# Kernel tuning notes

Measured on AMD Instinct MI355X. Metric: run time of the kernel, lower is better.

The kernel has to match this reference:

```python
import jax, jax.numpy as jnp
import numpy as np


def _lstm(x_seq, Wih, Whh, bih, bhh, hidden):
    """Single-layer batch_first LSTM, PyTorch gate order (i,f,g,o).
    x_seq: [B, T, D_in]. Returns (outputs [B, T, H], h_T [B, H])."""
    B = x_seq.shape[0]
    h0 = jnp.zeros((B, hidden), x_seq.dtype)
    c0 = jnp.zeros((B, hidden), x_seq.dtype)

    def step(carry, x_t):
        h, c = carry
        gates = x_t @ Wih.T + bih + h @ Whh.T + bhh  # [B, 4H]
        i, f, g, o = jnp.split(gates, 4, axis=-1)
        i = jax.nn.sigmoid(i)
        f = jax.nn.sigmoid(f)
        g = jnp.tanh(g)
        o = jax.nn.sigmoid(o)
        c = f * c + i * g
        h = o * jnp.tanh(c)
        return (h, c), h

    (hT, _), hs = jax.lax.scan(step, (h0, c0), jnp.swapaxes(x_seq, 0, 1))
    return jnp.swapaxes(hs, 0, 1), hT


def setup_inputs() -> dict:
    key = jax.random.key(0)
    ks = jax.random.split(key, 20)
    B, T = 4096, 140
    W = 0.1  # weight scale to keep gates out of saturation
    inp = {"x": jax.random.normal(ks[0], (B, 1, T), jnp.float32)}
    shapes = {
        "Wih_e1": (512, 1), "Whh_e1": (512, 128), "bih_e1": (512,), "bhh_e1": (512,),
        "Wih_e2": (256, 128), "Whh_e2": (256, 64), "bih_e2": (256,), "bhh_e2": (256,),
        "Wih_d1": (512, 64), "Whh_d1": (512, 128), "bih_d1": (512,), "bhh_d1": (512,),
        "Wih_d2": (4, 128), "Whh_d2": (4, 1), "bih_d2": (4,), "bhh_d2": (4,),
    }
    for i, (name, shp) in enumerate(shapes.items()):
        inp[name] = jax.random.normal(ks[i + 1], shp, jnp.float32) * W
    return inp


def reference(x, Wih_e1, Whh_e1, bih_e1, bhh_e1,
              Wih_e2, Whh_e2, bih_e2, bhh_e2,
              Wih_d1, Whh_d1, bih_d1, bhh_d1,
              Wih_d2, Whh_d2, bih_d2, bhh_d2):
    T = 140
    # x: [B,1,140] -> [B,140,1]
    x_enc = x[:, 0, :, None]
    _, h1 = _lstm(x_enc, Wih_e1, Whh_e1, bih_e1, bhh_e1, 128)  # h1: [B,128]
    # faithful to original bug: hn1 [1,B,128] fed as batch_first input (batch=1, seq=B)
    hn1_seq = h1[None, :, :]
    _, z = _lstm(hn1_seq, Wih_e2, Whh_e2, bih_e2, bhh_e2, 64)  # z: [1,64]
    dec_in = jnp.broadcast_to(z[:, None, :], (1, T, 64))
    out1, _ = _lstm(dec_in, Wih_d1, Whh_d1, bih_d1, bhh_d1, 128)  # [1,140,128]
    out2, _ = _lstm(out1, Wih_d2, Whh_d2, bih_d2, bhh_d2, 1)      # [1,140,1]
    recon = out2[..., 0][:, None, :]  # [1,1,140]
    return recon
```

## Files before the change

kernel.cpp:

```cpp
#include <hip/hip_runtime.h>
#include <hip/hip_bf16.h>


__device__ __forceinline__ float sigm(float x) {
  return 1.0f / (1.0f + __expf(-x));
}
__device__ __forceinline__ float tanh_fast(float x) {
  return 1.0f - 2.0f / (__expf(2.0f * x) + 1.0f);
}

template <int IMM>
__device__ __forceinline__ float qp(float v) {
  return __int_as_float(__builtin_amdgcn_ds_swizzle(__float_as_int(v), IMM));
}
#define QP_XOR1 0x80B1
#define QP_XOR2 0x804E
#define QP_ROT1 0x8093

__device__ __forceinline__ int swzc(int k) { return k + ((k >> 5) << 2); }

#define A_BB 16

__global__ __launch_bounds__(512, 2) void lstm_e1_kernel(
    const float* __restrict__ x,
    const float* __restrict__ Wih,
    const float* __restrict__ Whh,
    const float* __restrict__ bih,
    const float* __restrict__ bhh,
    float* __restrict__ h1_out)
{
  const int j    = threadIdx.x;
  const int lane = j & 63;
  const int w    = j >> 6;
  const int u    = w * 16 + (lane >> 2);
  const int q    = lane & 3;
  const int b0   = blockIdx.x * A_BB;

  __shared__ float Hs[2][A_BB][144];
  __shared__ float xs[2][A_BB];

  for (int i = j; i < A_BB * 144; i += 512) ((float*)Hs[0])[i] = 0.0f;
  if (j < A_BB) xs[0][j] = x[(b0 + j) * 140];

  float wr[4][32];
#pragma unroll
  for (int g = 0; g < 4; ++g)
#pragma unroll
    for (int k = 0; k < 32; k += 4)
      *(float4*)&wr[g][k] = *(const float4*)&Whh[(g * 128 + u) * 128 + q * 32 + k];

  float wih[4], bs[4];
#pragma unroll
  for (int g = 0; g < 4; ++g) {
    wih[g] = Wih[g * 128 + u];
    bs[g]  = bih[g * 128 + u] + bhh[g * 128 + u];
  }

  float c[4]  = {0.f, 0.f, 0.f, 0.f};
  float hr[4] = {0.f, 0.f, 0.f, 0.f};
  __syncthreads();

  int cur = 0;
  for (int t = 0; t < 140; ++t) {
    const int nxt = cur ^ 1;

    float R[4][4];
#pragma unroll
    for (int g = 0; g < 4; ++g)
#pragma unroll
      for (int i = 0; i < 4; ++i) R[g][i] = 0.0f;

#pragma unroll
    for (int s = 0; s < 4; ++s) {
      if (s) {
#pragma unroll
        for (int g = 0; g < 4; ++g)
#pragma unroll
          for (int i = 0; i < 4; ++i) R[g][i] = qp<QP_ROT1>(R[g][i]);
      }
      const int cch = (q - 1 - s) & 3;
      const float* hbase = &Hs[cur][cch * 4][q * 36];
#pragma unroll
      for (int i = 0; i < 4; ++i) {
        const float* hrow = hbase + i * 144;
#pragma unroll
        for (int kk = 0; kk < 8; ++kk) {
          const float4 hv = *(const float4*)&hrow[kk * 4];
#pragma unroll
          for (int g = 0; g < 4; ++g) {
            R[g][i] = __builtin_fmaf(wr[g][kk * 4 + 0], hv.x, R[g][i]);
            R[g][i] = __builtin_fmaf(wr[g][kk * 4 + 1], hv.y, R[g][i]);
            R[g][i] = __builtin_fmaf(wr[g][kk * 4 + 2], hv.z, R[g][i]);
            R[g][i] = __builtin_fmaf(wr[g][kk * 4 + 3], hv.w, R[g][i]);
          }
        }
      }
    }

    if (j < A_BB && (t + 1) < 140) xs[nxt][j] = x[(b0 + j) * 140 + t + 1];

    const float4 xv = *(const float4*)&xs[cur][q * 4];
    const float xa[4] = {xv.x, xv.y, xv.z, xv.w};
#pragma unroll
    for (int i = 0; i < 4; ++i) {
      const float gi = sigm(R[0][i] + __builtin_fmaf(wih[0], xa[i], bs[0]));
      const float gf = sigm(R[1][i] + __builtin_fmaf(wih[1], xa[i], bs[1]));
      const float gg = tanh_fast(R[2][i] + __builtin_fmaf(wih[2], xa[i], bs[2]));
      const float go = sigm(R[3][i] + __builtin_fmaf(wih[3], xa[i], bs[3]));
      c[i]  = gf * c[i] + gi * gg;
      hr[i] = go * tanh_fast(c[i]);
      Hs[nxt][q * 4 + i][swzc(u)] = hr[i];
    }
    __syncthreads();
    cur = nxt;
  }

#pragma unroll
  for (int i = 0; i < 4; ++i)
    h1_out[(b0 + q * 4 + i) * 128 + u] = hr[i];
}

__global__ __launch_bounds__(256, 1) void u_pre_kernel(
    const float* __restrict__ h1,
    const float* __restrict__ Wih,
    const float* __restrict__ bih,
    const float* __restrict__ bhh,
    float* __restrict__ Up)
{
  const int t = blockIdx.x;
  const int j = threadIdx.x;
  __shared__ float hs[128];
  if (j < 128) hs[j] = h1[t * 128 + j];
  __syncthreads();
  float acc = bih[j] + bhh[j];
#pragma unroll
  for (int k = 0; k < 128; k += 4) {
    const float4 hv = *(const float4*)&hs[k];
    const float4 wv = *(const float4*)&Wih[j * 128 + k];
    acc += wv.x * hv.x + wv.y * hv.y + wv.z * hv.z + wv.w * hv.w;
  }
  Up[t * 256 + (j & 63) * 4 + (j >> 6)] = acc;
}

__global__ __launch_bounds__(256, 1) void lstm_e2_scan_kernel(
    const float4* __restrict__ Up,
    const float* __restrict__ Whh,
    float* __restrict__ z_out)
{
  const int j = threadIdx.x;
  const int u = j >> 2;
  const int q = j & 3;

  __shared__ float hb[2][64];

  float wr[4][16];
#pragma unroll
  for (int g = 0; g < 4; ++g)
#pragma unroll
    for (int k = 0; k < 16; k += 4)
      *(float4*)&wr[g][k] = *(const float4*)&Whh[(g * 64 + u) * 64 + q * 16 + k];

  if (j < 64) hb[0][j] = 0.0f;
  float c = 0.0f, h = 0.0f;

  float4 U0 = Up[u];
  float4 U1 = Up[64 + u];
  __syncthreads();

  int cur = 0;
#pragma unroll 1
  for (int t = 0; t < 4096; t += 2) {
    {
      const int tp = (t + 2 < 4096) ? (t + 2) : 4095;
      const float4 Unew = Up[tp * 64 + u];
      float a0 = 0.f, a1 = 0.f, a2 = 0.f, a3 = 0.f;
#pragma unroll
      for (int kk = 0; kk < 4; ++kk) {
        const float4 hv = *(const float4*)&hb[cur][q * 16 + kk * 4];
        a0 = __builtin_fmaf(wr[0][kk*4+0], hv.x, a0); a0 = __builtin_fmaf(wr[0][kk*4+1], hv.y, a0);
        a0 = __builtin_fmaf(wr[0][kk*4+2], hv.z, a0); a0 = __builtin_fmaf(wr[0][kk*4+3], hv.w, a0);
        a1 = __builtin_fmaf(wr[1][kk*4+0], hv.x, a1); a1 = __builtin_fmaf(wr[1][kk*4+1], hv.y, a1);
        a1 = __builtin_fmaf(wr[1][kk*4+2], hv.z, a1); a1 = __builtin_fmaf(wr[1][kk*4+3], hv.w, a1);
        a2 = __builtin_fmaf(wr[2][kk*4+0], hv.x, a2); a2 = __builtin_fmaf(wr[2][kk*4+1], hv.y, a2);
        a2 = __builtin_fmaf(wr[2][kk*4+2], hv.z, a2); a2 = __builtin_fmaf(wr[2][kk*4+3], hv.w, a2);
        a3 = __builtin_fmaf(wr[3][kk*4+0], hv.x, a3); a3 = __builtin_fmaf(wr[3][kk*4+1], hv.y, a3);
        a3 = __builtin_fmaf(wr[3][kk*4+2], hv.z, a3); a3 = __builtin_fmaf(wr[3][kk*4+3], hv.w, a3);
      }
      a0 += qp<QP_XOR1>(a0); a0 += qp<QP_XOR2>(a0);
      a1 += qp<QP_XOR1>(a1); a1 += qp<QP_XOR2>(a1);
      a2 += qp<QP_XOR1>(a2); a2 += qp<QP_XOR2>(a2);
      a3 += qp<QP_XOR1>(a3); a3 += qp<QP_XOR2>(a3);
      const float gi = sigm(a0 + U0.x);
      const float gf = sigm(a1 + U0.y);
      const float gg = tanh_fast(a2 + U0.z);
      const float go = sigm(a3 + U0.w);
      c = gf * c + gi * gg;
      h = go * tanh_fast(c);
      if (q == 0) hb[cur ^ 1][u] = h;
      U0 = Unew;
      __syncthreads();
      cur ^= 1;
    }
    {
      const int tp = (t + 3 < 4096) ? (t + 3) : 4095;
      const float4 Unew = Up[tp * 64 + u];
      float a0 = 0.f, a1 = 0.f, a2 = 0.f, a3 = 0.f;
#pragma unroll
      for (int kk = 0; kk < 4; ++kk) {
        const float4 hv = *(const float4*)&hb[cur][q * 16 + kk * 4];
        a0 = __builtin_fmaf(wr[0][kk*4+0], hv.x, a0); a0 = __builtin_fmaf(wr[0][kk*4+1], hv.y, a0);
        a0 = __builtin_fmaf(wr[0][kk*4+2], hv.z, a0); a0 = __builtin_fmaf(wr[0][kk*4+3], hv.w, a0);
        a1 = __builtin_fmaf(wr[1][kk*4+0], hv.x, a1); a1 = __builtin_fmaf(wr[1][kk*4+1], hv.y, a1);
        a1 = __builtin_fmaf(wr[1][kk*4+2], hv.z, a1); a1 = __builtin_fmaf(wr[1][kk*4+3], hv.w, a1);
        a2 = __builtin_fmaf(wr[2][kk*4+0], hv.x, a2); a2 = __builtin_fmaf(wr[2][kk*4+1], hv.y, a2);
        a2 = __builtin_fmaf(wr[2][kk*4+2], hv.z, a2); a2 = __builtin_fmaf(wr[2][kk*4+3], hv.w, a2);
        a3 = __builtin_fmaf(wr[3][kk*4+0], hv.x, a3); a3 = __builtin_fmaf(wr[3][kk*4+1], hv.y, a3);
        a3 = __builtin_fmaf(wr[3][kk*4+2], hv.z, a3); a3 = __builtin_fmaf(wr[3][kk*4+3], hv.w, a3);
      }
      a0 += qp<QP_XOR1>(a0); a0 += qp<QP_XOR2>(a0);
      a1 += qp<QP_XOR1>(a1); a1 += qp<QP_XOR2>(a1);
      a2 += qp<QP_XOR1>(a2); a2 += qp<QP_XOR2>(a2);
      a3 += qp<QP_XOR1>(a3); a3 += qp<QP_XOR2>(a3);
      const float gi = sigm(a0 + U1.x);
      const float gf = sigm(a1 + U1.y);
      const float gg = tanh_fast(a2 + U1.z);
      const float go = sigm(a3 + U1.w);
      c = gf * c + gi * gg;
      h = go * tanh_fast(c);
      if (q == 0) hb[cur ^ 1][u] = h;
      U1 = Unew;
      __syncthreads();
      cur ^= 1;
    }
  }
  if (q == 0) z_out[u] = h;
}

__global__ __launch_bounds__(512, 1) void lstm_dec_kernel(
    const float* __restrict__ z,
    const float* __restrict__ Wih1,
    const float* __restrict__ Whh1,
    const float* __restrict__ bih1,
    const float* __restrict__ bhh1,
    const float* __restrict__ Wih2,
    const float* __restrict__ Whh2,
    const float* __restrict__ bih2,
    const float* __restrict__ bhh2,
    float* __restrict__ out)
{
  const int j = threadIdx.x;
  const int u = j >> 2;
  const int q = j & 3;

  __shared__ float hb[2][144];
  __shared__ float zs[64];

  if (j < 64) zs[j] = z[j];
  if (j < 144) hb[0][j] = 0.0f;
  __syncthreads();

  float wr[4][32];
#pragma unroll
  for (int g = 0; g < 4; ++g)
#pragma unroll
    for (int k = 0; k < 32; k += 4)
      *(float4*)&wr[g][k] = *(const float4*)&Whh1[(g * 128 + u) * 128 + q * 32 + k];

  float pre0[4];
#pragma unroll
  for (int g = 0; g < 4; ++g) {
    float acc = bih1[g * 128 + u] + bhh1[g * 128 + u];
#pragma unroll
    for (int k = 0; k < 64; k += 4) {
      const float4 zv = *(const float4*)&zs[k];
      const float4 wv = *(const float4*)&Wih1[(g * 128 + u) * 64 + k];
      acc += wv.x * zv.x + wv.y * zv.y + wv.z * zv.z + wv.w * zv.w;
    }
    pre0[g] = acc;
  }

  float w2[8] = {0,0,0,0,0,0,0,0}, b2[4] = {0,0,0,0}, wh2[4] = {0,0,0,0};
  if (j < 64) {
#pragma unroll
    for (int g = 0; g < 4; ++g) {
      w2[g * 2 + 0] = Wih2[g * 128 + 2 * j + 0];
      w2[g * 2 + 1] = Wih2[g * 128 + 2 * j + 1];
      b2[g]  = bih2[g] + bhh2[g];
      wh2[g] = Whh2[g];
    }
  }

  float c1 = 0.0f;
  float c2 = 0.0f, h2 = 0.0f;

  int cur = 0;
  for (int t = 0; t < 140; ++t) {
    float a0 = 0.f, a1 = 0.f, a2 = 0.f, a3 = 0.f;
#pragma unroll
    for (int kk = 0; kk < 8; ++kk) {
      const float4 hv = *(const float4*)&hb[cur][q * 36 + kk * 4];
      a0 = __builtin_fmaf(wr[0][kk*4+0], hv.x, a0); a0 = __builtin_fmaf(wr[0][kk*4+1], hv.y, a0);
      a0 = __builtin_fmaf(wr[0][kk*4+2], hv.z, a0); a0 = __builtin_fmaf(wr[0][kk*4+3], hv.w, a0);
      a1 = __builtin_fmaf(wr[1][kk*4+0], hv.x, a1); a1 = __builtin_fmaf(wr[1][kk*4+1], hv.y, a1);
      a1 = __builtin_fmaf(wr[1][kk*4+2], hv.z, a1); a1 = __builtin_fmaf(wr[1][kk*4+3], hv.w, a1);
      a2 = __builtin_fmaf(wr[2][kk*4+0], hv.x, a2); a2 = __builtin_fmaf(wr[2][kk*4+1], hv.y, a2);
      a2 = __builtin_fmaf(wr[2][kk*4+2], hv.z, a2); a2 = __builtin_fmaf(wr[2][kk*4+3], hv.w, a2);
      a3 = __builtin_fmaf(wr[3][kk*4+0], hv.x, a3); a3 = __builtin_fmaf(wr[3][kk*4+1], hv.y, a3);
      a3 = __builtin_fmaf(wr[3][kk*4+2], hv.z, a3); a3 = __builtin_fmaf(wr[3][kk*4+3], hv.w, a3);
    }
    a0 += qp<QP_XOR1>(a0); a0 += qp<QP_XOR2>(a0);
    a1 += qp<QP_XOR1>(a1); a1 += qp<QP_XOR2>(a1);
    a2 += qp<QP_XOR1>(a2); a2 += qp<QP_XOR2>(a2);
    a3 += qp<QP_XOR1>(a3); a3 += qp<QP_XOR2>(a3);

    const float gi = sigm(a0 + pre0[0]);
    const float gf = sigm(a1 + pre0[1]);
    const float gg = tanh_fast(a2 + pre0[2]);
    const float go = sigm(a3 + pre0[3]);
    c1 = gf * c1 + gi * gg;
    const float h1v = go * tanh_fast(c1);
    if (q == 0) hb[cur ^ 1][swzc(u)] = h1v;
    __syncthreads();
    cur ^= 1;

    if (j < 64) {
      const float hA = hb[cur][swzc(2 * j)];
      const float hB = hb[cur][swzc(2 * j + 1)];
      float p0 = hA * w2[0] + hB * w2[1];
      float p1 = hA * w2[2] + hB * w2[3];
      float p2 = hA * w2[4] + hB * w2[5];
      float p3 = hA * w2[6] + hB * w2[7];
#pragma unroll
      for (int s = 1; s < 64; s <<= 1) {
        p0 += __shfl_xor(p0, s);
        p1 += __shfl_xor(p1, s);
        p2 += __shfl_xor(p2, s);
        p3 += __shfl_xor(p3, s);
      }
      const float g2i = sigm(p0 + b2[0] + wh2[0] * h2);
      const float g2f = sigm(p1 + b2[1] + wh2[1] * h2);
      const float g2g = tanh_fast(p2 + b2[2] + wh2[2] * h2);
      const float g2o = sigm(p3 + b2[3] + wh2[3] * h2);
      c2 = g2f * c2 + g2i * g2g;
      h2 = g2o * tanh_fast(c2);
      if (j == 0) out[t] = h2;
    }
  }
}

extern "C" void kernel_launch(void* const* d_in, const int* in_sizes, int n_in,
                              void* d_out, int out_size, void* d_ws, size_t ws_size,
                              hipStream_t stream) {
  const float* x      = (const float*)d_in[0];
  const float* Wih_e1 = (const float*)d_in[1];
  const float* Whh_e1 = (const float*)d_in[2];
  const float* bih_e1 = (const float*)d_in[3];
  const float* bhh_e1 = (const float*)d_in[4];
  const float* Wih_e2 = (const float*)d_in[5];
  const float* Whh_e2 = (const float*)d_in[6];
  const float* bih_e2 = (const float*)d_in[7];
  const float* bhh_e2 = (const float*)d_in[8];
  const float* Wih_d1 = (const float*)d_in[9];
  const float* Whh_d1 = (const float*)d_in[10];
  const float* bih_d1 = (const float*)d_in[11];
  const float* bhh_d1 = (const float*)d_in[12];
  const float* Wih_d2 = (const float*)d_in[13];
  const float* Whh_d2 = (const float*)d_in[14];
  const float* bih_d2 = (const float*)d_in[15];
  const float* bhh_d2 = (const float*)d_in[16];

  float* out = (float*)d_out;

  float* h1 = (float*)d_ws;
  float* Up = h1 + 4096 * 128;
  float* zb = Up + 4096 * 256;

  lstm_e1_kernel<<<4096 / A_BB, 512, 0, stream>>>(x, Wih_e1, Whh_e1, bih_e1, bhh_e1, h1);
  u_pre_kernel<<<4096, 256, 0, stream>>>(h1, Wih_e2, bih_e2, bhh_e2, Up);
  lstm_e2_scan_kernel<<<1, 256, 0, stream>>>((const float4*)Up, Whh_e2, zb);
  lstm_dec_kernel<<<1, 512, 0, stream>>>(zb, Wih_d1, Whh_d1, bih_d1, bhh_d1,
                                         Wih_d2, Whh_d2, bih_d2, bhh_d2, out);
}
```

Before: 3.907 ms.

## Use DPP cross-lane reductions and widen the serial encoder-2 scan to 8 lanes per unit

Replaces the ds_swizzle quad permutes with DPP row moves in all kernels. The 4096-step encoder-2 scan now runs 512 threads, with 8 lanes per hidden unit doing 8 FMAs each, and reduces with a three-level DPP tree. This shortens the per-step dependent chain on the serial critical path, at the cost of one extra reduction level and wider barriers. The decoder's second layer switches from a 64-lane shuffle reduction over all gates to a 16-lane DPP reduction per gate, exchanged through a small shared array. It also leaves a dead, unused gate computation in place.

```diff
diff --git a/kernel.cpp b/kernel.cpp
--- a/kernel.cpp
+++ b/kernel.cpp
@@ -9,13 +9,16 @@
   return 1.0f - 2.0f / (__expf(2.0f * x) + 1.0f);
 }
 
-template <int IMM>
-__device__ __forceinline__ float qp(float v) {
-  return __int_as_float(__builtin_amdgcn_ds_swizzle(__float_as_int(v), IMM));
-}
-#define QP_XOR1 0x80B1
-#define QP_XOR2 0x804E
-#define QP_ROT1 0x8093
+template <int CTRL>
+__device__ __forceinline__ float dppmv(float v) {
+  return __int_as_float(__builtin_amdgcn_update_dpp(
+      0, __float_as_int(v), CTRL, 0xF, 0xF, true));
+}
+#define DPP_XOR1   0xB1
+#define DPP_XOR2   0x4E
+#define DPP_ROT1   0x93
+#define DPP_HMIRR  0x141
+#define DPP_MIRR   0x140
 
 __device__ __forceinline__ int swzc(int k) { return k + ((k >> 5) << 2); }
 
@@ -76,7 +79,7 @@
 #pragma unroll
         for (int g = 0; g < 4; ++g)
 #pragma unroll
-          for (int i = 0; i < 4; ++i) R[g][i] = qp<QP_ROT1>(R[g][i]);
+          for (int i = 0; i < 4; ++i) R[g][i] = dppmv<DPP_ROT1>(R[g][i]);
       }
       const int cch = (q - 1 - s) & 3;
       const float* hbase = &Hs[cur][cch * 4][q * 36];
@@ -142,23 +145,23 @@
   Up[t * 256 + (j & 63) * 4 + (j >> 6)] = acc;
 }
 
-__global__ __launch_bounds__(256, 1) void lstm_e2_scan_kernel(
+__global__ __launch_bounds__(512, 1) void lstm_e2_scan_kernel(
     const float4* __restrict__ Up,
     const float* __restrict__ Whh,
     float* __restrict__ z_out)
 {
   const int j = threadIdx.x;
-  const int u = j >> 2;
-  const int q = j & 3;
+  const int u = j >> 3;
+  const int o = j & 7;
 
   __shared__ float hb[2][64];
 
-  float wr[4][16];
-#pragma unroll
-  for (int g = 0; g < 4; ++g)
-#pragma unroll
-    for (int k = 0; k < 16; k += 4)
-      *(float4*)&wr[g][k] = *(const float4*)&Whh[(g * 64 + u) * 64 + q * 16 + k];
+  float wr[4][8];
+#pragma unroll
+  for (int g = 0; g < 4; ++g) {
+    *(float4*)&wr[g][0] = *(const float4*)&Whh[(g * 64 + u) * 64 + o * 8];
+    *(float4*)&wr[g][4] = *(const float4*)&Whh[(g * 64 + u) * 64 + o * 8 + 4];
+  }
 
   if (j < 64) hb[0][j] = 0.0f;
   float c = 0.0f, h = 0.0f;
@@ -170,70 +173,51 @@
   int cur = 0;
 #pragma unroll 1
   for (int t = 0; t < 4096; t += 2) {
-    {
-      const int tp = (t + 2 < 4096) ? (t + 2) : 4095;
+#pragma unroll
+    for (int half = 0; half < 2; ++half) {
+      const int tp = (t + 2 + half < 4096) ? (t + 2 + half) : 4095;
       const float4 Unew = Up[tp * 64 + u];
-      float a0 = 0.f, a1 = 0.f, a2 = 0.f, a3 = 0.f;
-#pragma unroll
-      for (int kk = 0; kk < 4; ++kk) {
-        const float4 hv = *(const float4*)&hb[cur][q * 16 + kk * 4];
-        a0 = __builtin_fmaf(wr[0][kk*4+0], hv.x, a0); a0 = __builtin_fmaf(wr[0][kk*4+1], hv.y, a0);
-        a0 = __builtin_fmaf(wr[0][kk*4+2], hv.z, a0); a0 = __builtin_fmaf(wr[0][kk*4+3], hv.w, a0);
-        a1 = __builtin_fmaf(wr[1][kk*4+0], hv.x, a1); a1 = __builtin_fmaf(wr[1][kk*4+1], hv.y, a1);
-        a1 = __builtin_fmaf(wr[1][kk*4+2], hv.z, a1); a1 = __builtin_fmaf(wr[1][kk*4+3], hv.w, a1);
-        a2 = __builtin_fmaf(wr[2][kk*4+0], hv.x, a2); a2 = __builtin_fmaf(wr[2][kk*4+1], hv.y, a2);
-        a2 = __builtin_fmaf(wr[2][kk*4+2], hv.z, a2); a2 = __builtin_fmaf(wr[2][kk*4+3], hv.w, a2);
-        a3 = __builtin_fmaf(wr[3][kk*4+0], hv.x, a3); a3 = __builtin_fmaf(wr[3][kk*4+1], hv.y, a3);
-        a3 = __builtin_fmaf(wr[3][kk*4+2], hv.z, a3); a3 = __builtin_fmaf(wr[3][kk*4+3], hv.w, a3);
-      }
-      a0 += qp<QP_XOR1>(a0); a0 += qp<QP_XOR2>(a0);
-      a1 += qp<QP_XOR1>(a1); a1 += qp<QP_XOR2>(a1);
-      a2 += qp<QP_XOR1>(a2); a2 += qp<QP_XOR2>(a2);
-      a3 += qp<QP_XOR1>(a3); a3 += qp<QP_XOR2>(a3);
-      const float gi = sigm(a0 + U0.x);
-      const float gf = sigm(a1 + U0.y);
-      const float gg = tanh_fast(a2 + U0.z);
-      const float go = sigm(a3 + U0.w);
+      const float4 Ucur = half ? U1 : U0;
+
+      const float4 hv0 = *(const float4*)&hb[cur][o * 8];
+      const float4 hv1 = *(const float4*)&hb[cur][o * 8 + 4];
+      float a0, a1, a2, a3;
+      a0 = wr[0][0] * hv0.x; a1 = wr[1][0] * hv0.x; a2 = wr[2][0] * hv0.x; a3 = wr[3][0] * hv0.x;
+      a0 = __builtin_fmaf(wr[0][1], hv0.y, a0); a1 = __builtin_fmaf(wr[1][1], hv0.y, a1);
+      a2 = __builtin_fmaf(wr[2][1], hv0.y, a2); a3 = __builtin_fmaf(wr[3][1], hv0.y, a3);
+      a0 = __builtin_fmaf(wr[0][2], hv0.z, a0); a1 = __builtin_fmaf(wr[1][2], hv0.z, a1);
+      a2 = __builtin_fmaf(wr[2][2], hv0.z, a2); a3 = __builtin_fmaf(wr[3][2], hv0.z, a3);
+      a0 = __builtin_fmaf(wr[0][3], hv0.w, a0); a1 = __builtin_fmaf(wr[1][3], hv0.w, a1);
+      a2 = __builtin_fmaf(wr[2][3], hv0.w, a2); a3 = __builtin_fmaf(wr[3][3], hv0.w, a3);
+      a0 = __builtin_fmaf(wr[0][4], hv1.x, a0); a1 = __builtin_fmaf(wr[1][4], hv1.x, a1);
+      a2 = __builtin_fmaf(wr[2][4], hv1.x, a2); a3 = __builtin_fmaf(wr[3][4], hv1.x, a3);
+      a0 = __builtin_fmaf(wr[0][5], hv1.y, a0); a1 = __builtin_fmaf(wr[1][5], hv1.y, a1);
+      a2 = __builtin_fmaf(wr[2][5], hv1.y, a2); a3 = __builtin_fmaf(wr[3][5], hv1.y, a3);
+      a0 = __builtin_fmaf(wr[0][6], hv1.z, a0); a1 = __builtin_fmaf(wr[1][6], hv1.z, a1);
+      a2 = __builtin_fmaf(wr[2][6], hv1.z, a2); a3 = __builtin_fmaf(wr[3][6], hv1.z, a3);
+      a0 = __builtin_fmaf(wr[0][7], hv1.w, a0); a1 = __builtin_fmaf(wr[1][7], hv1.w, a1);
+      a2 = __builtin_fmaf(wr[2][7], hv1.w, a2); a3 = __builtin_fmaf(wr[3][7], hv1.w, a3);
+
+      a0 += dppmv<DPP_XOR1>(a0);  a1 += dppmv<DPP_XOR1>(a1);
+      a2 += dppmv<DPP_XOR1>(a2);  a3 += dppmv<DPP_XOR1>(a3);
+      a0 += dppmv<DPP_XOR2>(a0);  a1 += dppmv<DPP_XOR2>(a1);
+      a2 += dppmv<DPP_XOR2>(a2);  a3 += dppmv<DPP_XOR2>(a3);
+      a0 += dppmv<DPP_HMIRR>(a0); a1 += dppmv<DPP_HMIRR>(a1);
+      a2 += dppmv<DPP_HMIRR>(a2); a3 += dppmv<DPP_HMIRR>(a3);
+
+      const float gi = sigm(a0 + Ucur.x);
+      const float gf = sigm(a1 + Ucur.y);
+      const float gg = tanh_fast(a2 + Ucur.z);
+      const float go = sigm(a3 + Ucur.w);
       c = gf * c + gi * gg;
       h = go * tanh_fast(c);
-      if (q == 0) hb[cur ^ 1][u] = h;
-      U0 = Unew;
+      if (o == 0) hb[cur ^ 1][u] = h;
+      if (half) U1 = Unew; else U0 = Unew;
       __syncthreads();
       cur ^= 1;
     }
-    {
-      const int tp = (t + 3 < 4096) ? (t + 3) : 4095;
-      const float4 Unew = Up[tp * 64 + u];
-      float a0 = 0.f, a1 = 0.f, a2 = 0.f, a3 = 0.f;
-#pragma unroll
-      for (int kk = 0; kk < 4; ++kk) {
-        const float4 hv = *(const float4*)&hb[cur][q * 16 + kk * 4];
-        a0 = __builtin_fmaf(wr[0][kk*4+0], hv.x, a0); a0 = __builtin_fmaf(wr[0][kk*4+1], hv.y, a0);
-        a0 = __builtin_fmaf(wr[0][kk*4+2], hv.z, a0); a0 = __builtin_fmaf(wr[0][kk*4+3], hv.w, a0);
-        a1 = __builtin_fmaf(wr[1][kk*4+0], hv.x, a1); a1 = __builtin_fmaf(wr[1][kk*4+1], hv.y, a1);
-        a1 = __builtin_fmaf(wr[1][kk*4+2], hv.z, a1); a1 = __builtin_fmaf(wr[1][kk*4+3], hv.w, a1);
-        a2 = __builtin_fmaf(wr[2][kk*4+0], hv.x, a2); a2 = __builtin_fmaf(wr[2][kk*4+1], hv.y, a2);
-        a2 = __builtin_fmaf(wr[2][kk*4+2], hv.z, a2); a2 = __builtin_fmaf(wr[2][kk*4+3], hv.w, a2);
-        a3 = __builtin_fmaf(wr[3][kk*4+0], hv.x, a3); a3 = __builtin_fmaf(wr[3][kk*4+1], hv.y, a3);
-        a3 = __builtin_fmaf(wr[3][kk*4+2], hv.z, a3); a3 = __builtin_fmaf(wr[3][kk*4+3], hv.w, a3);
-      }
-      a0 += qp<QP_XOR1>(a0); a0 += qp<QP_XOR2>(a0);
-      a1 += qp<QP_XOR1>(a1); a1 += qp<QP_XOR2>(a1);
-      a2 += qp<QP_XOR1>(a2); a2 += qp<QP_XOR2>(a2);
-      a3 += qp<QP_XOR1>(a3); a3 += qp<QP_XOR2>(a3);
-      const float gi = sigm(a0 + U1.x);
-      const float gf = sigm(a1 + U1.y);
-      const float gg = tanh_fast(a2 + U1.z);
-      const float go = sigm(a3 + U1.w);
-      c = gf * c + gi * gg;
-      h = go * tanh_fast(c);
-      if (q == 0) hb[cur ^ 1][u] = h;
-      U1 = Unew;
-      __syncthreads();
-      cur ^= 1;
-    }
-  }
-  if (q == 0) z_out[u] = h;
+  }
+  if (o == 0) z_out[u] = h;
 }
 
 __global__ __launch_bounds__(512, 1) void lstm_dec_kernel(
@@ -254,6 +238,7 @@
 
   __shared__ float hb[2][144];
   __shared__ float zs[64];
+  __shared__ float act4[4];
 
   if (j < 64) zs[j] = z[j];
   if (j < 144) hb[0][j] = 0.0f;
@@ -279,15 +264,15 @@
     pre0[g] = acc;
   }
 
-  float w2[8] = {0,0,0,0,0,0,0,0}, b2[4] = {0,0,0,0}, wh2[4] = {0,0,0,0};
+  const int g2  = j >> 4;
+  const int i16 = j & 15;
+  float w2d[8] = {0,0,0,0,0,0,0,0};
+  float b2 = 0.0f, wh2 = 0.0f;
   if (j < 64) {
 #pragma unroll
-    for (int g = 0; g < 4; ++g) {
-      w2[g * 2 + 0] = Wih2[g * 128 + 2 * j + 0];
-      w2[g * 2 + 1] = Wih2[g * 128 + 2 * j + 1];
-      b2[g]  = bih2[g] + bhh2[g];
-      wh2[g] = Whh2[g];
-    }
+    for (int e = 0; e < 8; ++e) w2d[e] = Wih2[g2 * 128 + i16 * 8 + e];
+    b2  = bih2[g2] + bhh2[g2];
+    wh2 = Whh2[g2];
   }
 
   float c1 = 0.0f;
@@ -308,10 +293,10 @@
       a3 = __builtin_fmaf(wr[3][kk*4+0], hv.x, a3); a3 = __builtin_fmaf(wr[3][kk*4+1], hv.y, a3);
       a3 = __builtin_fmaf(wr[3][kk*4+2], hv.z, a3); a3 = __builtin_fmaf(wr[3][kk*4+3], hv.w, a3);
     }
-    a0 += qp<QP_XOR1>(a0); a0 += qp<QP_XOR2>(a0);
-    a1 += qp<QP_XOR1>(a1); a1 += qp<QP_XOR2>(a1);
-    a2 += qp<QP_XOR1>(a2); a2 += qp<QP_XOR2>(a2);
-    a3 += qp<QP_XOR1>(a3); a3 += qp<QP_XOR2>(a3);
+    a0 += dppmv<DPP_XOR1>(a0); a0 += dppmv<DPP_XOR2>(a0);
+    a1 += dppmv<DPP_XOR1>(a1); a1 += dppmv<DPP_XOR2>(a1);
+    a2 += dppmv<DPP_XOR1>(a2); a2 += dppmv<DPP_XOR2>(a2);
+    a3 += dppmv<DPP_XOR1>(a3); a3 += dppmv<DPP_XOR2>(a3);
 
     const float gi = sigm(a0 + pre0[0]);
     const float gf = sigm(a1 + pre0[1]);
@@ -324,25 +309,31 @@
     cur ^= 1;
 
     if (j < 64) {
-      const float hA = hb[cur][swzc(2 * j)];
-      const float hB = hb[cur][swzc(2 * j + 1)];
-      float p0 = hA * w2[0] + hB * w2[1];
-      float p1 = hA * w2[2] + hB * w2[3];
-      float p2 = hA * w2[4] + hB * w2[5];
-      float p3 = hA * w2[6] + hB * w2[7];
-#pragma unroll
-      for (int s = 1; s < 64; s <<= 1) {
-        p0 += __shfl_xor(p0, s);
-        p1 += __shfl_xor(p1, s);
-        p2 += __shfl_xor(p2, s);
-        p3 += __shfl_xor(p3, s);
-      }
-      const float g2i = sigm(p0 + b2[0] + wh2[0] * h2);
-      const float g2f = sigm(p1 + b2[1] + wh2[1] * h2);
-      const float g2g = tanh_fast(p2 + b2[2] + wh2[2] * h2);
-      const float g2o = sigm(p3 + b2[3] + wh2[3] * h2);
-      c2 = g2f * c2 + g2i * g2g;
-      h2 = g2o * tanh_fast(c2);
+      const int kb = i16 * 8;
+      const float4 hA = *(const float4*)&hb[cur][swzc(kb)];
+      const float4 hB = *(const float4*)&hb[cur][swzc(kb) + 4];
+      float p = hA.x * w2d[0];
+      p = __builtin_fmaf(hA.y, w2d[1], p);
+      p = __builtin_fmaf(hA.z, w2d[2], p);
+      p = __builtin_fmaf(hA.w, w2d[3], p);
+      p = __builtin_fmaf(hB.x, w2d[4], p);
+      p = __builtin_fmaf(hB.y, w2d[5], p);
+      p = __builtin_fmaf(hB.z, w2d[6], p);
+      p = __builtin_fmaf(hB.w, w2d[7], p);
+      p += dppmv<DPP_XOR1>(p);
+      p += dppmv<DPP_XOR2>(p);
+      p += dppmv<DPP_HMIRR>(p);
+      p += dppmv<DPP_MIRR>(p);
+      if (i16 == 0) act4[g2] = p;
+      const float4 acts = *(const float4*)&act4[0];
+      const float d2i = sigm(acts.x + b2 * 0.0f + (bih2[0] + bhh2[0]) * 0.0f + (acts.x * 0.0f) + (bih2[0]*0.0f) + ( (bih2[0]+bhh2[0]) ) + wh2 * 0.0f + Whh2[0] * h2);
+      (void)d2i;
+      const float gi2 = sigm(acts.x + (bih2[0] + bhh2[0]) + Whh2[0] * h2);
+      const float gf2 = sigm(acts.y + (bih2[1] + bhh2[1]) + Whh2[1] * h2);
+      const float gg2 = tanh_fast(acts.z + (bih2[2] + bhh2[2]) + Whh2[2] * h2);
+      const float go2 = sigm(acts.w + (bih2[3] + bhh2[3]) + Whh2[3] * h2);
+      c2 = gf2 * c2 + gi2 * gg2;
+      h2 = go2 * tanh_fast(c2);
       if (j == 0) out[t] = h2;
     }
   }
@@ -377,7 +368,7 @@
 
   lstm_e1_kernel<<<4096 / A_BB, 512, 0, stream>>>(x, Wih_e1, Whh_e1, bih_e1, bhh_e1, h1);
   u_pre_kernel<<<4096, 256, 0, stream>>>(h1, Wih_e2, bih_e2, bhh_e2, Up);
-  lstm_e2_scan_kernel<<<1, 256, 0, stream>>>((const float4*)Up, Whh_e2, zb);
+  lstm_e2_scan_kernel<<<1, 512, 0, stream>>>((const float4*)Up, Whh_e2, zb);
   lstm_dec_kernel<<<1, 512, 0, stream>>>(zb, Wih_d1, Whh_d1, bih_d1, bhh_d1,
                                          Wih_d2, Whh_d2, bih_d2, bhh_d2, out);
 }
```

New measurement: 3.912 ms. About the same (+0.1%).
